# Optimization experiments

Hardware: AMD Instinct MI355X
Metric: run time of the kernel (lower is better)

## Reference

```python
import jax, jax.numpy as jnp
import numpy as np

B, T, C = 2, 2048, 2048
NH, NKV = 16, 16
HD = C // NH            # 128
GATE_CH = 32
ROPE_BASE = 10000.0


def setup_inputs() -> dict:
    key = jax.random.key(0)
    ks = jax.random.split(key, 8)
    x = jax.random.normal(ks[0], (B, T, C), jnp.float32)
    ve = jax.random.normal(ks[1], (B, T, C), jnp.float32)
    # RoPE tables: half-dim rotation, shape broadcastable to [B, T, H, HD//2]
    d2 = HD // 2
    inv_freq = 1.0 / (ROPE_BASE ** (jnp.arange(d2, dtype=jnp.float32) / d2))
    angles = jnp.arange(T, dtype=jnp.float32)[:, None] * inv_freq[None, :]  # [T, d2]
    cos = jnp.cos(angles)[None, :, None, :]  # [1, T, 1, d2]
    sin = jnp.sin(angles)[None, :, None, :]
    s = 0.02
    Wq = jax.random.normal(ks[2], (C, NH * HD), jnp.float32) * s
    Wk = jax.random.normal(ks[3], (C, NKV * HD), jnp.float32) * s
    Wv = jax.random.normal(ks[4], (C, NKV * HD), jnp.float32) * s
    Wgate = jax.random.normal(ks[5], (GATE_CH, NKV), jnp.float32) * s
    Wproj = jax.random.normal(ks[6], (NH * HD, C), jnp.float32) * s
    return {"x": x, "ve": ve, "cos": cos, "sin": sin,
            "Wq": Wq, "Wk": Wk, "Wv": Wv, "Wgate": Wgate, "Wproj": Wproj}


def _apply_rotary(x, cos, sin):
    d = x.shape[3] // 2
    x1, x2 = x[..., :d], x[..., d:]
    return jnp.concatenate([x1 * cos + x2 * sin, x1 * -sin + x2 * cos], axis=3)


def _rms_norm(x):
    return x * jax.lax.rsqrt(jnp.mean(x * x, axis=-1, keepdims=True) + 1e-6)


def reference(x, ve, cos, sin, Wq, Wk, Wv, Wgate, Wproj):
    b, t, c = x.shape
    q = (x @ Wq).reshape(b, t, NH, HD)
    k = (x @ Wk).reshape(b, t, NKV, HD)
    v = (x @ Wv).reshape(b, t, NKV, HD)
    # value-embedding gate
    ve_r = ve.reshape(b, t, NKV, HD)
    gate = 2.0 * jax.nn.sigmoid(x[..., :GATE_CH] @ Wgate)  # [B, T, NKV]
    v = v + gate[..., None] * ve_r
    # RoPE then QK-RMSNorm
    q = _rms_norm(_apply_rotary(q, cos, sin))
    k = _rms_norm(_apply_rotary(k, cos, sin))
    # causal attention, scale = 1/sqrt(head_dim)
    scale = 1.0 / np.sqrt(HD).astype(np.float32)
    scores = jnp.einsum('bqhd,bkhd->bhqk', q, k) * scale
    causal = jnp.tril(jnp.ones((t, t), dtype=bool))
    scores = jnp.where(causal, scores, jnp.finfo(scores.dtype).min)
    probs = jax.nn.softmax(scores, axis=-1)
    y = jnp.einsum('bhqk,bkhd->bqhd', probs, v)
    y = y.reshape(b, t, NH * HD)
    return y @ Wproj
```

## Files before the change

kernel.cpp:

```cpp
#include <hip/hip_runtime.h>
#include <stdint.h>

typedef short bf16x8 __attribute__((ext_vector_type(8)));
typedef float f32x4 __attribute__((ext_vector_type(4)));

#define ASYNC16(g, l) __builtin_amdgcn_global_load_lds( \
    (const __attribute__((address_space(1))) unsigned int*)(g), \
    (__attribute__((address_space(3))) unsigned int*)(l), 16, 0, 0)

__device__ __forceinline__ float bf2f(short u) {
  union { unsigned int i; float f; } v;
  v.i = ((unsigned int)(unsigned short)u) << 16;
  return v.f;
}
__device__ __forceinline__ short f2bf(float f) {
  union { float f; unsigned int i; } v;
  v.f = f;
  return (short)(unsigned short)((v.i + 0x8000u) >> 16);
}
__device__ __forceinline__ float ldf(const void* p, long i, int isbf) {
  return isbf ? bf2f(((const short*)p)[i]) : ((const float*)p)[i];
}

__global__ void detect_dtype(const short* __restrict__ x, int* __restrict__ flag) {
  if (threadIdx.x == 0 && blockIdx.x == 0) {
    int cnt = 0;
    for (int i = 0; i < 128; ++i) {
      int e = (((unsigned short)x[i]) >> 7) & 0xFF;
      if (e >= 110 && e <= 136) ++cnt;
    }
    *flag = (cnt >= 120) ? 1 : 0;
  }
}

__global__ __launch_bounds__(256) void convert_x(
    const void* __restrict__ xin, short* __restrict__ xb, const int* __restrict__ flag) {
  long i = (long)blockIdx.x * 2048 + (long)threadIdx.x * 8;
  if (*flag) {
    *(bf16x8*)(xb + i) = *(const bf16x8*)((const short*)xin + i);
  } else {
    const float* xf = (const float*)xin;
    short tmp[8];
    #pragma unroll
    for (int j = 0; j < 8; ++j) tmp[j] = f2bf(xf[i + j]);
    *(bf16x8*)(xb + i) = *(bf16x8*)tmp;
  }
}

__global__ __launch_bounds__(256) void transpose_w(
    const void* __restrict__ S0, short* __restrict__ D0,
    const void* __restrict__ S1, short* __restrict__ D1,
    const void* __restrict__ S2, short* __restrict__ D2,
    const int* __restrict__ flag)
{
  int z = blockIdx.z;
  const void* S = (z == 0) ? S0 : (z == 1) ? S1 : S2;
  short* D = (z == 0) ? D0 : (z == 1) ? D1 : D2;
  int isbf = *flag;
  __shared__ short tile[32][33];
  int c0 = blockIdx.x * 32, r0 = blockIdx.y * 32;
  int tx = threadIdx.x, ty = threadIdx.y;
  #pragma unroll
  for (int i = 0; i < 4; ++i)
    tile[ty + 8*i][tx] = f2bf(ldf(S, (long)(r0 + ty + 8*i) * 2048 + c0 + tx, isbf));
  __syncthreads();
  #pragma unroll
  for (int i = 0; i < 4; ++i)
    D[(long)(c0 + ty + 8*i) * 2048 + r0 + tx] = tile[tx][ty + 8*i];
}

__global__ __launch_bounds__(256) void transpose_v(
    const short* __restrict__ Vr, short* __restrict__ Vt)
{
  __shared__ short tile[32][33];
  int bh = blockIdx.z;
  int b = bh >> 4, h = bh & 15;
  int t0 = blockIdx.x * 32, d0 = blockIdx.y * 32;
  int tx = threadIdx.x, ty = threadIdx.y;
  #pragma unroll
  for (int i = 0; i < 4; ++i)
    tile[ty + 8*i][tx] = Vr[(long)(b*2048 + t0 + ty + 8*i) * 2048 + h*128 + d0 + tx];
  __syncthreads();
  #pragma unroll
  for (int i = 0; i < 4; ++i)
    Vt[((long)bh * 128 + d0 + ty + 8*i) * 2048 + t0 + tx] = tile[tx][ty + 8*i];
}

template<typename OutT>
__global__ __launch_bounds__(256) void gemm_bt(
    const short* __restrict__ A,
    const short* __restrict__ B0, const short* __restrict__ B1, const short* __restrict__ B2,
    OutT* __restrict__ C0, OutT* __restrict__ C1, OutT* __restrict__ C2,
    int M, int N, int K)
{
  int z = blockIdx.z;
  const short* Bt = (z == 0) ? B0 : (z == 1) ? B1 : B2;
  OutT* C = (z == 0) ? C0 : (z == 1) ? C1 : C2;

  int m0 = blockIdx.y * 128, n0 = blockIdx.x * 128;
  int tid = threadIdx.x;
  int lane = tid & 63, w = tid >> 6;
  int quad = lane >> 4, l16 = lane & 15;
  int wm = w >> 1, wn = w & 1;

  __shared__ short As[128][64];
  __shared__ short Bs[128][64];

  f32x4 zero4 = {0.f, 0.f, 0.f, 0.f};
  f32x4 acc[4][4];
  #pragma unroll
  for (int i = 0; i < 4; ++i)
    #pragma unroll
    for (int j = 0; j < 4; ++j) acc[i][j] = zero4;

  int r8 = lane >> 3;
  int srow = w * 32 + r8;
  int scol = ((lane & 7) ^ r8) * 8;

  for (int k0 = 0; k0 < K; k0 += 64) {
    #pragma unroll
    for (int i = 0; i < 4; ++i) {
      ASYNC16(A  + (long)(m0 + srow + i*8) * K + k0 + scol, &As[w*32 + i*8][0]);
      ASYNC16(Bt + (long)(n0 + srow + i*8) * K + k0 + scol, &Bs[w*32 + i*8][0]);
    }
    __syncthreads();
    #pragma unroll
    for (int kt = 0; kt < 2; ++kt) {
      int po = ((kt*4 + quad) ^ (l16 & 7)) * 8;
      bf16x8 af[4], bfr[4];
      #pragma unroll
      for (int i = 0; i < 4; ++i)
        af[i] = *(const bf16x8*)&As[wm*64 + i*16 + l16][po];
      #pragma unroll
      for (int j = 0; j < 4; ++j)
        bfr[j] = *(const bf16x8*)&Bs[wn*64 + j*16 + l16][po];
      #pragma unroll
      for (int i = 0; i < 4; ++i)
        #pragma unroll
        for (int j = 0; j < 4; ++j)
          acc[i][j] = __builtin_amdgcn_mfma_f32_16x16x32_bf16(af[i], bfr[j], acc[i][j], 0, 0, 0);
    }
    __syncthreads();
  }

  #pragma unroll
  for (int i = 0; i < 4; ++i)
    #pragma unroll
    for (int j = 0; j < 4; ++j) {
      int row = m0 + wm*64 + i*16 + quad*4;
      int col = n0 + wn*64 + j*16 + l16;
      #pragma unroll
      for (int r = 0; r < 4; ++r) {
        float v = acc[i][j][r];
        if constexpr (sizeof(OutT) == 4)
          C[(long)(row + r) * N + col] = v;
        else
          C[(long)(row + r) * N + col] = (OutT)f2bf(v);
      }
    }
}

__global__ __launch_bounds__(256) void pointwise(
    const short* __restrict__ xb, const void* __restrict__ ve,
    const void* __restrict__ cosb, const void* __restrict__ sinb,
    const void* __restrict__ Wg, const int* __restrict__ flag,
    short* __restrict__ Qr, short* __restrict__ Kr, short* __restrict__ Vr)
{
  int row = blockIdx.x;
  int tid = threadIdx.x;
  int isbf = *flag;
  __shared__ float xg[32];
  __shared__ float gates[16];
  if (tid < 32) xg[tid] = bf2f(xb[(long)row * 2048 + tid]);
  __syncthreads();
  if (tid < 16) {
    float g = 0.f;
    #pragma unroll
    for (int i = 0; i < 32; ++i) g += xg[i] * ldf(Wg, i*16 + tid, isbf);
    gates[tid] = 2.0f / (1.0f + __expf(-g));
  }
  __syncthreads();
  #pragma unroll
  for (int it = 0; it < 8; ++it) {
    int idx = it * 256 + tid;
    int h = idx >> 7;
    long p = (long)row * 2048 + idx;
    Vr[p] = f2bf(bf2f(Vr[p]) + gates[h] * ldf(ve, p, isbf));
  }
  int lane = tid & 63, w = tid >> 6;
  int t = row & 2047;
  #pragma unroll
  for (int it = 0; it < 8; ++it) {
    int unit = it * 4 + w;
    short* P = (unit < 16) ? Qr : Kr;
    int h = unit & 15;
    long base = (long)row * 2048 + h * 128;
    float x1 = bf2f(P[base + lane]);
    float x2 = bf2f(P[base + lane + 64]);
    float c = ldf(cosb, t*64 + lane, isbf);
    float s = ldf(sinb, t*64 + lane, isbf);
    float r1 = x1 * c + x2 * s;
    float r2 = -x1 * s + x2 * c;
    float ss = r1*r1 + r2*r2;
    #pragma unroll
    for (int off = 32; off; off >>= 1) ss += __shfl_xor(ss, off);
    float rn = rsqrtf(ss * (1.0f/128.0f) + 1e-6f);
    P[base + lane]      = f2bf(r1 * rn);
    P[base + lane + 64] = f2bf(r2 * rn);
  }
}

#define FL_C1 0.12751741f
#define FL_C2 16.321698f

__global__ __launch_bounds__(256) void flash(
    const short* __restrict__ Q, const short* __restrict__ K,
    const short* __restrict__ Vt, short* __restrict__ Y)
{
  int bx = blockIdx.x;
  int bh = blockIdx.y;
  int b = bh >> 4, h = bh & 15;
  int tid = threadIdx.x;
  int lane = tid & 63, w = tid >> 6;
  int quad = lane >> 4, l16 = lane & 15;

  __shared__ short Ks[2][64*128];
  __shared__ short Vts[2][128*64];
  __shared__ short Ps[4][16*72];

  int qtA = bx, qtB = 31 - bx;
  int nA = qtA + 1, nB = qtB + 1;
  int total = nA + nB;

  int kkey = tid >> 4;
  int klo  = (tid & 15) ^ (kkey & 7);
  int vd   = tid >> 3;
  int vlo  = (tid & 7) ^ (vd & 7);
  const short* Kbase = K + (long)(b*2048 + kkey) * 2048 + h*128 + klo*8;
  const short* Vbase = Vt + ((long)bh*128 + vd) * 2048 + vlo*8;

  f32x4 zero4 = {0.f, 0.f, 0.f, 0.f};
  f32x4 o[8];
  float l_i[4];
  bf16x8 qf[4];
  bf16x8 ones;
  #pragma unroll
  for (int j = 0; j < 8; ++j) ones[j] = (short)0x3F80;

  auto stage = [&](int tt, int buf) {
    int tl = (tt < nA) ? tt : tt - nA;
    long ko = (long)tl * 64 * 2048;
    int  vo = tl * 64;
    #pragma unroll
    for (int i = 0; i < 4; ++i)
      ASYNC16(Kbase + ko + (long)i*16*2048, &Ks[buf][(i*16 + w*4)*128]);
    #pragma unroll
    for (int i = 0; i < 4; ++i)
      ASYNC16(Vbase + vo + (long)i*32*2048, &Vts[buf][(i*32 + w*8)*64]);
  };
  auto loadQ = [&](int qt) {
    const short* Qb = Q + (long)(b*2048 + qt*64 + w*16 + l16) * 2048 + h*128;
    #pragma unroll
    for (int kt = 0; kt < 4; ++kt)
      qf[kt] = *(const bf16x8*)(Qb + kt*32 + quad*8);
  };
  auto flushO = [&](int qt) {
    #pragma unroll
    for (int r = 0; r < 4; ++r) {
      float inv = 1.0f / fmaxf(l_i[r], 1e-30f);
      short* yp = Y + (long)(b*2048 + qt*64 + w*16 + quad*4 + r) * 2048 + h*128;
      #pragma unroll
      for (int c8 = 0; c8 < 8; ++c8)
        yp[c8*16 + l16] = f2bf(o[c8][r] * inv);
    }
  };

  #pragma unroll
  for (int c = 0; c < 8; ++c) o[c] = zero4;
  #pragma unroll
  for (int r = 0; r < 4; ++r) l_i[r] = 0.f;
  loadQ(qtA);
  stage(0, 0);

  int qt = qtA, n_seg = nA, segbase = 0;
  for (int tt = 0; tt < total; ++tt) {
    int buf = tt & 1;
    asm volatile("s_waitcnt vmcnt(0)" ::: "memory");
    __builtin_amdgcn_s_barrier();
    if (tt + 1 < total) stage(tt + 1, buf ^ 1);
    if (tt == nA) {
      flushO(qtA);
      loadQ(qtB);
      #pragma unroll
      for (int c = 0; c < 8; ++c) o[c] = zero4;
      #pragma unroll
      for (int r = 0; r < 4; ++r) l_i[r] = 0.f;
      qt = qtB; n_seg = nB; segbase = nA;
    }
    int tloc = tt - segbase;
    int kv0 = tloc * 64;

    f32x4 s[4];
    #pragma unroll
    for (int c = 0; c < 4; ++c) {
      f32x4 acc = zero4;
      #pragma unroll
      for (int kt = 0; kt < 4; ++kt) {
        int po = ((kt*4 + quad) ^ (l16 & 7)) * 8;
        bf16x8 kf = *(const bf16x8*)&Ks[buf][(c*16 + l16)*128 + po];
        acc = __builtin_amdgcn_mfma_f32_16x16x32_bf16(qf[kt], kf, acc, 0, 0, 0);
      }
      s[c] = acc;
    }

    bool domask = (tloc == n_seg - 1);
    int qgb = qt*64 + w*16 + quad*4;
    #pragma unroll
    for (int c = 0; c < 4; ++c) {
      int kg = kv0 + c*16 + l16;
      #pragma unroll
      for (int r = 0; r < 4; ++r) {
        float t = s[c][r] * FL_C1 - FL_C2;
        if (domask && kg > qgb + r) t = -1000.0f;
        float pv = exp2f(t);
        Ps[w][(quad*4 + r)*72 + c*16 + l16] = f2bf(pv);
      }
    }
    asm volatile("s_waitcnt lgkmcnt(0)" ::: "memory");
    bf16x8 pa0 = *(const bf16x8*)&Ps[w][l16*72 + quad*8];
    bf16x8 pa1 = *(const bf16x8*)&Ps[w][l16*72 + 32 + quad*8];

    f32x4 racc = __builtin_amdgcn_mfma_f32_16x16x32_bf16(pa0, ones, zero4, 0, 0, 0);
    racc = __builtin_amdgcn_mfma_f32_16x16x32_bf16(pa1, ones, racc, 0, 0, 0);
    #pragma unroll
    for (int r = 0; r < 4; ++r) l_i[r] += racc[r];

    #pragma unroll
    for (int c8 = 0; c8 < 8; ++c8) {
      int po0 = ((0*4 + quad) ^ (l16 & 7)) * 8;
      int po1 = ((1*4 + quad) ^ (l16 & 7)) * 8;
      bf16x8 v0 = *(const bf16x8*)&Vts[buf][(c8*16 + l16)*64 + po0];
      bf16x8 v1 = *(const bf16x8*)&Vts[buf][(c8*16 + l16)*64 + po1];
      o[c8] = __builtin_amdgcn_mfma_f32_16x16x32_bf16(pa0, v0, o[c8], 0, 0, 0);
      o[c8] = __builtin_amdgcn_mfma_f32_16x16x32_bf16(pa1, v1, o[c8], 0, 0, 0);
    }
  }
  flushO(qtB);
}

extern "C" void kernel_launch(void* const* d_in, const int* in_sizes, int n_in,
                              void* d_out, int out_size, void* d_ws, size_t ws_size,
                              hipStream_t stream) {
  const void* x    = d_in[0];
  const void* ve   = d_in[1];
  const void* cosb = d_in[2];
  const void* sinb = d_in[3];
  const void* Wq   = d_in[4];
  const void* Wk   = d_in[5];
  const void* Wv   = d_in[6];
  const void* Wg   = d_in[7];
  const void* Wp   = d_in[8];
  float* out = (float*)d_out;

  int*   flag = (int*)d_ws;
  short* base = (short*)d_ws + 256;
  short* wt0 = base;
  short* wtk = base + 4194304L;
  short* wtv = base + 8388608L;
  short* Vt  = base + 4194304L;
  short* xb  = base + 12582912L;
  short* Y   = base + 12582912L;
  short* Qr  = base + 20971520L;
  short* Kr  = base + 29360128L;
  short* Vr  = base + 37748736L;

  detect_dtype<<<1, 64, 0, stream>>>((const short*)x, flag);
  convert_x<<<4096, 256, 0, stream>>>(x, xb, flag);
  transpose_w<<<dim3(64, 64, 3), dim3(32, 8), 0, stream>>>(Wq, wt0, Wk, wtk, Wv, wtv, flag);
  gemm_bt<short><<<dim3(16, 32, 3), 256, 0, stream>>>(xb, wt0, wtk, wtv, Qr, Kr, Vr, 4096, 2048, 2048);
  transpose_w<<<dim3(64, 64, 1), dim3(32, 8), 0, stream>>>(Wp, wt0, Wp, wt0, Wp, wt0, flag);
  pointwise<<<dim3(4096), 256, 0, stream>>>(xb, ve, cosb, sinb, Wg, flag, Qr, Kr, Vr);
  transpose_v<<<dim3(64, 4, 32), dim3(32, 8), 0, stream>>>(Vr, Vt);
  flash<<<dim3(16, 32), 256, 0, stream>>>(Qr, Kr, Vt, Y);
  gemm_bt<float><<<dim3(16, 32, 1), 256, 0, stream>>>(Y, wt0, wt0, wt0, out, out, out, 4096, 2048, 2048);
}
```

Before: 476.9 us.

## Add 256x256 ping-pong GEMM for QKV, vectorize gate update, prioritize MFMA in flash

Adds a new 512-thread GEMM kernel with 256x256 output tiles, split double-buffered LDS staging of half-K chunks, and barrier-interleaved async loads with s_setprio around MFMA bursts. The QKV projection now uses it in place of the 128-tile GEMM. The pointwise value-gate update is vectorized to 8-element loads and stores, and the flash kernel raises wave priority around its MFMA sections. The large tile raises register and LDS pressure and restricts occupancy to two blocks per CU.

```diff
diff --git a/kernel.cpp b/kernel.cpp
--- a/kernel.cpp
+++ b/kernel.cpp
@@ -152,6 +152,161 @@
       #pragma unroll
       for (int r = 0; r < 4; ++r) {
         float v = acc[i][j][r];
+        if constexpr (sizeof(OutT) == 4)
+          C[(long)(row + r) * N + col] = v;
+        else
+          C[(long)(row + r) * N + col] = (OutT)f2bf(v);
+      }
+    }
+}
+
+template<typename OutT>
+__global__ __launch_bounds__(512, 2) void gemm256(
+    const short* __restrict__ A,
+    const short* __restrict__ B0, const short* __restrict__ B1, const short* __restrict__ B2,
+    OutT* __restrict__ C0, OutT* __restrict__ C1, OutT* __restrict__ C2,
+    int M, int N, int K)
+{
+  int z = blockIdx.z;
+  const short* Bt = (z == 0) ? B0 : (z == 1) ? B1 : B2;
+  OutT* C = (z == 0) ? C0 : (z == 1) ? C1 : C2;
+
+  int m0 = blockIdx.y * 256, n0 = blockIdx.x * 256;
+  int tid = threadIdx.x;
+  int lane = tid & 63, w = tid >> 6;
+  int quad = lane >> 4, l16 = lane & 15;
+  int wm = w >> 2, wn = w & 3;
+
+  __shared__ short Ag[2][2][128*64];
+  __shared__ short Bg[2][2][128*64];
+
+  f32x4 zero4 = {0.f, 0.f, 0.f, 0.f};
+  f32x4 acc[8][4];
+  #pragma unroll
+  for (int i = 0; i < 8; ++i)
+    #pragma unroll
+    for (int j = 0; j < 4; ++j) acc[i][j] = zero4;
+
+  int l8 = lane >> 3, o = lane & 7, lo = o ^ l8;
+  int rowb = w*16 + 2*l8 + (lo >> 2);
+  int colb = (lo & 3) * 8;
+  const short* Ab = A  + (long)(m0 + rowb) * K + colb;
+  const short* Bb = Bt + (long)(n0 + rowb) * K + colb;
+
+  int hl = l16 >> 1;
+  int phys = ((((l16 & 1) << 2) + quad) ^ hl) * 8;
+  int rdA = (wm*64 + hl)*64 + phys;
+  int rdB = (wn*32 + hl)*64 + phys;
+
+  int NT = K >> 6;
+
+  ASYNC16(Ab,             &Ag[0][0][(w*8)*64]);
+  ASYNC16(Ab + 128L*K,    &Ag[0][0][(64 + w*8)*64]);
+  ASYNC16(Bb,             &Bg[0][0][(w*8)*64]);
+  ASYNC16(Bb + 128L*K,    &Bg[0][0][(64 + w*8)*64]);
+  ASYNC16(Ab + 32,        &Ag[0][1][(w*8)*64]);
+  ASYNC16(Ab + 32 + 128L*K, &Ag[0][1][(64 + w*8)*64]);
+  ASYNC16(Bb + 32,        &Bg[0][1][(w*8)*64]);
+  ASYNC16(Bb + 32 + 128L*K, &Bg[0][1][(64 + w*8)*64]);
+  asm volatile("s_waitcnt vmcnt(4)" ::: "memory");
+  __builtin_amdgcn_s_barrier();
+
+  bf16x8 am[8], b0, b1;
+
+  for (int t = 0; t < NT; ++t) {
+    int db = t & 1, sdb = db ^ 1;
+    long kn = (long)(t + 1) * 64;
+    bool st = (t + 1 < NT);
+
+    #pragma unroll
+    for (int mf = 0; mf < 8; ++mf)
+      am[mf] = *(const bf16x8*)&Ag[db][0][rdA + mf*512];
+    b0 = *(const bf16x8*)&Bg[db][0][rdB];
+    b1 = *(const bf16x8*)&Bg[db][0][rdB + 512];
+    if (st) {
+      ASYNC16(Ab + kn,            &Ag[sdb][0][(w*8)*64]);
+      ASYNC16(Ab + kn + 128L*K,   &Ag[sdb][0][(64 + w*8)*64]);
+    }
+    __builtin_amdgcn_s_barrier();
+    __builtin_amdgcn_s_setprio(1);
+    #pragma unroll
+    for (int mf = 0; mf < 8; ++mf)
+      acc[mf][0] = __builtin_amdgcn_mfma_f32_16x16x32_bf16(am[mf], b0, acc[mf][0], 0, 0, 0);
+    #pragma unroll
+    for (int mf = 0; mf < 8; ++mf)
+      acc[mf][1] = __builtin_amdgcn_mfma_f32_16x16x32_bf16(am[mf], b1, acc[mf][1], 0, 0, 0);
+    __builtin_amdgcn_s_setprio(0);
+    __builtin_amdgcn_s_barrier();
+
+    b0 = *(const bf16x8*)&Bg[db][0][rdB + 2*512];
+    b1 = *(const bf16x8*)&Bg[db][0][rdB + 3*512];
+    if (st) {
+      ASYNC16(Bb + kn,            &Bg[sdb][0][(w*8)*64]);
+      ASYNC16(Bb + kn + 128L*K,   &Bg[sdb][0][(64 + w*8)*64]);
+    }
+    __builtin_amdgcn_s_barrier();
+    __builtin_amdgcn_s_setprio(1);
+    #pragma unroll
+    for (int mf = 0; mf < 8; ++mf)
+      acc[mf][2] = __builtin_amdgcn_mfma_f32_16x16x32_bf16(am[mf], b0, acc[mf][2], 0, 0, 0);
+    #pragma unroll
+    for (int mf = 0; mf < 8; ++mf)
+      acc[mf][3] = __builtin_amdgcn_mfma_f32_16x16x32_bf16(am[mf], b1, acc[mf][3], 0, 0, 0);
+    __builtin_amdgcn_s_setprio(0);
+    if (st) asm volatile("s_waitcnt vmcnt(4)" ::: "memory");
+    else    asm volatile("s_waitcnt vmcnt(0)" ::: "memory");
+    __builtin_amdgcn_s_barrier();
+
+    #pragma unroll
+    for (int mf = 0; mf < 8; ++mf)
+      am[mf] = *(const bf16x8*)&Ag[db][1][rdA + mf*512];
+    b0 = *(const bf16x8*)&Bg[db][1][rdB];
+    b1 = *(const bf16x8*)&Bg[db][1][rdB + 512];
+    if (st) {
+      ASYNC16(Ab + kn + 32,          &Ag[sdb][1][(w*8)*64]);
+      ASYNC16(Ab + kn + 32 + 128L*K, &Ag[sdb][1][(64 + w*8)*64]);
+    }
+    __builtin_amdgcn_s_barrier();
+    __builtin_amdgcn_s_setprio(1);
+    #pragma unroll
+    for (int mf = 0; mf < 8; ++mf)
+      acc[mf][0] = __builtin_amdgcn_mfma_f32_16x16x32_bf16(am[mf], b0, acc[mf][0], 0, 0, 0);
+    #pragma unroll
+    for (int mf = 0; mf < 8; ++mf)
+      acc[mf][1] = __builtin_amdgcn_mfma_f32_16x16x32_bf16(am[mf], b1, acc[mf][1], 0, 0, 0);
+    __builtin_amdgcn_s_setprio(0);
+    __builtin_amdgcn_s_barrier();
+
+    b0 = *(const bf16x8*)&Bg[db][1][rdB + 2*512];
+    b1 = *(const bf16x8*)&Bg[db][1][rdB + 3*512];
+    if (st) {
+      ASYNC16(Bb + kn + 32,          &Bg[sdb][1][(w*8)*64]);
+      ASYNC16(Bb + kn + 32 + 128L*K, &Bg[sdb][1][(64 + w*8)*64]);
+    }
+    __builtin_amdgcn_s_barrier();
+    __builtin_amdgcn_s_setprio(1);
+    #pragma unroll
+    for (int mf = 0; mf < 8; ++mf)
+      acc[mf][2] = __builtin_amdgcn_mfma_f32_16x16x32_bf16(am[mf], b0, acc[mf][2], 0, 0, 0);
+    #pragma unroll
+    for (int mf = 0; mf < 8; ++mf)
+      acc[mf][3] = __builtin_amdgcn_mfma_f32_16x16x32_bf16(am[mf], b1, acc[mf][3], 0, 0, 0);
+    __builtin_amdgcn_s_setprio(0);
+    if (st) {
+      asm volatile("s_waitcnt vmcnt(4)" ::: "memory");
+      __builtin_amdgcn_s_barrier();
+    }
+  }
+
+  #pragma unroll
+  for (int mf = 0; mf < 8; ++mf)
+    #pragma unroll
+    for (int nf = 0; nf < 4; ++nf) {
+      int row = m0 + wm*128 + mf*16 + quad*4;
+      int col = n0 + wn*64 + nf*16 + l16;
+      #pragma unroll
+      for (int r = 0; r < 4; ++r) {
+        float v = acc[mf][nf][r];
         if constexpr (sizeof(OutT) == 4)
           C[(long)(row + r) * N + col] = v;
         else
@@ -180,12 +335,27 @@
     gates[tid] = 2.0f / (1.0f + __expf(-g));
   }
   __syncthreads();
-  #pragma unroll
-  for (int it = 0; it < 8; ++it) {
-    int idx = it * 256 + tid;
+  {
+    int idx = tid * 8;
     int h = idx >> 7;
     long p = (long)row * 2048 + idx;
-    Vr[p] = f2bf(bf2f(Vr[p]) + gates[h] * ldf(ve, p, isbf));
+    float g = gates[h];
+    bf16x8 vv = *(bf16x8*)(Vr + p);
+    short tmp[8];
+    if (isbf) {
+      bf16x8 vb = *(const bf16x8*)((const short*)ve + p);
+      #pragma unroll
+      for (int j = 0; j < 8; ++j) tmp[j] = f2bf(bf2f(vv[j]) + g * bf2f(vb[j]));
+    } else {
+      const float* vf = (const float*)ve;
+      f32x4 a = *(const f32x4*)(vf + p);
+      f32x4 b2 = *(const f32x4*)(vf + p + 4);
+      #pragma unroll
+      for (int j = 0; j < 4; ++j) tmp[j]     = f2bf(bf2f(vv[j])     + g * a[j]);
+      #pragma unroll
+      for (int j = 0; j < 4; ++j) tmp[j + 4] = f2bf(bf2f(vv[j + 4]) + g * b2[j]);
+    }
+    *(bf16x8*)(Vr + p) = *(bf16x8*)tmp;
   }
   int lane = tid & 63, w = tid >> 6;
   int t = row & 2047;
@@ -247,16 +417,16 @@
   #pragma unroll
   for (int j = 0; j < 8; ++j) ones[j] = (short)0x3F80;
 
-  auto stage = [&](int tt, int buf) {
+  auto stage = [&](int tt, int bufp) {
     int tl = (tt < nA) ? tt : tt - nA;
     long ko = (long)tl * 64 * 2048;
     int  vo = tl * 64;
     #pragma unroll
     for (int i = 0; i < 4; ++i)
-      ASYNC16(Kbase + ko + (long)i*16*2048, &Ks[buf][(i*16 + w*4)*128]);
+      ASYNC16(Kbase + ko + (long)i*16*2048, &Ks[bufp][(i*16 + w*4)*128]);
     #pragma unroll
     for (int i = 0; i < 4; ++i)
-      ASYNC16(Vbase + vo + (long)i*32*2048, &Vts[buf][(i*32 + w*8)*64]);
+      ASYNC16(Vbase + vo + (long)i*32*2048, &Vts[bufp][(i*32 + w*8)*64]);
   };
   auto loadQ = [&](int qt) {
     const short* Qb = Q + (long)(b*2048 + qt*64 + w*16 + l16) * 2048 + h*128;
@@ -301,6 +471,7 @@
     int kv0 = tloc * 64;
 
     f32x4 s[4];
+    __builtin_amdgcn_s_setprio(1);
     #pragma unroll
     for (int c = 0; c < 4; ++c) {
       f32x4 acc = zero4;
@@ -312,6 +483,7 @@
       }
       s[c] = acc;
     }
+    __builtin_amdgcn_s_setprio(0);
 
     bool domask = (tloc == n_seg - 1);
     int qgb = qt*64 + w*16 + quad*4;
@@ -330,6 +502,7 @@
     bf16x8 pa0 = *(const bf16x8*)&Ps[w][l16*72 + quad*8];
     bf16x8 pa1 = *(const bf16x8*)&Ps[w][l16*72 + 32 + quad*8];
 
+    __builtin_amdgcn_s_setprio(1);
     f32x4 racc = __builtin_amdgcn_mfma_f32_16x16x32_bf16(pa0, ones, zero4, 0, 0, 0);
     racc = __builtin_amdgcn_mfma_f32_16x16x32_bf16(pa1, ones, racc, 0, 0, 0);
     #pragma unroll
@@ -344,6 +517,7 @@
       o[c8] = __builtin_amdgcn_mfma_f32_16x16x32_bf16(pa0, v0, o[c8], 0, 0, 0);
       o[c8] = __builtin_amdgcn_mfma_f32_16x16x32_bf16(pa1, v1, o[c8], 0, 0, 0);
     }
+    __builtin_amdgcn_s_setprio(0);
   }
   flushO(qtB);
 }
@@ -377,7 +551,7 @@
   detect_dtype<<<1, 64, 0, stream>>>((const short*)x, flag);
   convert_x<<<4096, 256, 0, stream>>>(x, xb, flag);
   transpose_w<<<dim3(64, 64, 3), dim3(32, 8), 0, stream>>>(Wq, wt0, Wk, wtk, Wv, wtv, flag);
-  gemm_bt<short><<<dim3(16, 32, 3), 256, 0, stream>>>(xb, wt0, wtk, wtv, Qr, Kr, Vr, 4096, 2048, 2048);
+  gemm256<short><<<dim3(8, 16, 3), 512, 0, stream>>>(xb, wt0, wtk, wtv, Qr, Kr, Vr, 4096, 2048, 2048);
   transpose_w<<<dim3(64, 64, 1), dim3(32, 8), 0, stream>>>(Wp, wt0, Wp, wt0, Wp, wt0, flag);
   pointwise<<<dim3(4096), 256, 0, stream>>>(xb, ve, cosb, sinb, Wg, flag, Qr, Kr, Vr);
   transpose_v<<<dim3(64, 4, 32), dim3(32, 8), 0, stream>>>(Vr, Vt);
```

After: 469.9 us. No clear change (-1.5%).

## Remap blocks per XCD for L2 locality, vectorize gate update, add MFMA priority

Applied to the files above, without the earlier changes.

The GEMM and flash-attention block indices are remapped so that blocks sharing A/B tiles or the same batch-head land on the same XCD, which improves L2 reuse on the multi-die GPU. The value-gate update in the RoPE/norm kernel now handles 8 contiguous elements per thread with vector loads and stores instead of strided scalar accesses. s_setprio is raised around the MFMA sections in flash attention to favour matrix issue across waves. The remapping hardcodes grid shapes (16 columns, 8 XCDs), so it is only correct for these dimensions.

```diff
diff --git a/kernel.cpp b/kernel.cpp
--- a/kernel.cpp
+++ b/kernel.cpp
@@ -97,7 +97,12 @@
   const short* Bt = (z == 0) ? B0 : (z == 1) ? B1 : B2;
   OutT* C = (z == 0) ? C0 : (z == 1) ? C1 : C2;
 
-  int m0 = blockIdx.y * 128, n0 = blockIdx.x * 128;
+  int d = blockIdx.y * 16 + blockIdx.x;
+  int xcd = d & 7, ci = d >> 3;
+  int bx = (xcd & 1) * 8 + (ci & 7);
+  int by = (xcd >> 1) * 8 + (ci >> 3);
+  int m0 = by * 128, n0 = bx * 128;
+
   int tid = threadIdx.x;
   int lane = tid & 63, w = tid >> 6;
   int quad = lane >> 4, l16 = lane & 15;
@@ -180,12 +185,27 @@
     gates[tid] = 2.0f / (1.0f + __expf(-g));
   }
   __syncthreads();
-  #pragma unroll
-  for (int it = 0; it < 8; ++it) {
-    int idx = it * 256 + tid;
+  {
+    int idx = tid * 8;
     int h = idx >> 7;
     long p = (long)row * 2048 + idx;
-    Vr[p] = f2bf(bf2f(Vr[p]) + gates[h] * ldf(ve, p, isbf));
+    float g = gates[h];
+    bf16x8 vv = *(bf16x8*)(Vr + p);
+    short tmp[8];
+    if (isbf) {
+      bf16x8 vb = *(const bf16x8*)((const short*)ve + p);
+      #pragma unroll
+      for (int j = 0; j < 8; ++j) tmp[j] = f2bf(bf2f(vv[j]) + g * bf2f(vb[j]));
+    } else {
+      const float* vf = (const float*)ve;
+      f32x4 a = *(const f32x4*)(vf + p);
+      f32x4 b2 = *(const f32x4*)(vf + p + 4);
+      #pragma unroll
+      for (int j = 0; j < 4; ++j) tmp[j]     = f2bf(bf2f(vv[j])     + g * a[j]);
+      #pragma unroll
+      for (int j = 0; j < 4; ++j) tmp[j + 4] = f2bf(bf2f(vv[j + 4]) + g * b2[j]);
+    }
+    *(bf16x8*)(Vr + p) = *(bf16x8*)tmp;
   }
   int lane = tid & 63, w = tid >> 6;
   int t = row & 2047;
@@ -217,8 +237,10 @@
     const short* __restrict__ Q, const short* __restrict__ K,
     const short* __restrict__ Vt, short* __restrict__ Y)
 {
-  int bx = blockIdx.x;
-  int bh = blockIdx.y;
+  int d = blockIdx.y * 16 + blockIdx.x;
+  int xcd = d & 7, ci = d >> 3;
+  int bx = ci & 15;
+  int bh = xcd * 4 + (ci >> 4);
   int b = bh >> 4, h = bh & 15;
   int tid = threadIdx.x;
   int lane = tid & 63, w = tid >> 6;
@@ -247,16 +269,16 @@
   #pragma unroll
   for (int j = 0; j < 8; ++j) ones[j] = (short)0x3F80;
 
-  auto stage = [&](int tt, int buf) {
+  auto stage = [&](int tt, int bufp) {
     int tl = (tt < nA) ? tt : tt - nA;
     long ko = (long)tl * 64 * 2048;
     int  vo = tl * 64;
     #pragma unroll
     for (int i = 0; i < 4; ++i)
-      ASYNC16(Kbase + ko + (long)i*16*2048, &Ks[buf][(i*16 + w*4)*128]);
+      ASYNC16(Kbase + ko + (long)i*16*2048, &Ks[bufp][(i*16 + w*4)*128]);
     #pragma unroll
     for (int i = 0; i < 4; ++i)
-      ASYNC16(Vbase + vo + (long)i*32*2048, &Vts[buf][(i*32 + w*8)*64]);
+      ASYNC16(Vbase + vo + (long)i*32*2048, &Vts[bufp][(i*32 + w*8)*64]);
   };
   auto loadQ = [&](int qt) {
     const short* Qb = Q + (long)(b*2048 + qt*64 + w*16 + l16) * 2048 + h*128;
@@ -301,6 +323,7 @@
     int kv0 = tloc * 64;
 
     f32x4 s[4];
+    __builtin_amdgcn_s_setprio(1);
     #pragma unroll
     for (int c = 0; c < 4; ++c) {
       f32x4 acc = zero4;
@@ -312,6 +335,7 @@
       }
       s[c] = acc;
     }
+    __builtin_amdgcn_s_setprio(0);
 
     bool domask = (tloc == n_seg - 1);
     int qgb = qt*64 + w*16 + quad*4;
@@ -330,6 +354,7 @@
     bf16x8 pa0 = *(const bf16x8*)&Ps[w][l16*72 + quad*8];
     bf16x8 pa1 = *(const bf16x8*)&Ps[w][l16*72 + 32 + quad*8];
 
+    __builtin_amdgcn_s_setprio(1);
     f32x4 racc = __builtin_amdgcn_mfma_f32_16x16x32_bf16(pa0, ones, zero4, 0, 0, 0);
     racc = __builtin_amdgcn_mfma_f32_16x16x32_bf16(pa1, ones, racc, 0, 0, 0);
     #pragma unroll
@@ -344,6 +369,7 @@
       o[c8] = __builtin_amdgcn_mfma_f32_16x16x32_bf16(pa0, v0, o[c8], 0, 0, 0);
       o[c8] = __builtin_amdgcn_mfma_f32_16x16x32_bf16(pa1, v1, o[c8], 0, 0, 0);
     }
+    __builtin_amdgcn_s_setprio(0);
   }
   flushO(qtB);
 }
```

New measurement: 456.7 us. 1.04x faster.
